# Performance work log

Hardware: AMD Instinct MI355X
Metric: run time of the kernel (lower is better)

The kernel has to match this reference:

```python
import jax, jax.numpy as jnp
import numpy as np

N = 4096   # query tokens
M = 4096   # key/value tokens
D = 512    # embedding_dim


def setup_inputs() -> dict:
    key = jax.random.key(0)
    kq, kk, kv = jax.random.split(key, 3)
    return {
        "query": jax.random.normal(kq, (N, D), dtype=jnp.float32),
        "key": jax.random.normal(kk, (M, D), dtype=jnp.float32),
        "value": jax.random.normal(kv, (M, D), dtype=jnp.float32),
    }


def reference(query, key, value):
    # scores = Q K^T  (no 1/sqrt(d) scaling in the original module)
    attention_scores = jnp.einsum("nd,md->nm", query, key)  # [N, M]
    attention_probs = jax.nn.softmax(attention_scores, axis=-1)  # [N, M]
    output = jnp.einsum("nm,md->nd", attention_probs, value)  # [N, D]
    return (output, attention_probs)
```

## Files before the change

kernel.cpp:

```cpp
#include <hip/hip_runtime.h>
#include <hip/hip_bf16.h>
#include <stdint.h>

#define N_Q 4096
#define N_K 4096
#define DIM 512

typedef float f32x4 __attribute__((ext_vector_type(4)));
typedef __bf16 bf16x8 __attribute__((ext_vector_type(8)));
typedef unsigned short u16x4 __attribute__((ext_vector_type(4)));
typedef int i32x4 __attribute__((ext_vector_type(4)));

__device__ __forceinline__ f32x4 mfma_bf16(bf16x8 a, bf16x8 b, f32x4 c) {
  return __builtin_amdgcn_mfma_f32_16x16x32_bf16(a, b, c, 0, 0, 0);
}

__device__ __forceinline__ i32x4 mfma_i8(i32x4 a, i32x4 b, i32x4 c) {
  return __builtin_amdgcn_mfma_i32_16x16x64_i8(a, b, c, 0, 0, 0);
}

__device__ __forceinline__ void gload16(const void* g, void* l) {
  __builtin_amdgcn_global_load_lds((const __attribute__((address_space(1))) void*)g,
                                   (__attribute__((address_space(3))) void*)l,
                                   16, 0, 0);
}

__device__ __forceinline__ void split4(const f32x4 v, u16x4& h, u16x4& l) {
#pragma unroll
  for (int i = 0; i < 4; ++i) {
    float f = v[i];
    uint32_t u = __builtin_bit_cast(uint32_t, f);
    uint32_t hb = (u + 0x8000u) & 0xffff0000u;
    float hf = __builtin_bit_cast(float, hb);
    float lf = f - hf;
    h[i] = (unsigned short)(hb >> 16);
    l[i] = (unsigned short)(__builtin_bit_cast(uint32_t, lf) >> 16);
  }
}

__device__ __forceinline__ unsigned short bf16r(float f) {
  uint32_t u = __builtin_bit_cast(uint32_t, f);
  return (unsigned short)((u + 0x8000u) >> 16);
}

__global__ __launch_bounds__(256) void prep_kernel(const float* __restrict__ Q,
                                                   const float* __restrict__ K,
                                                   const float* __restrict__ V,
                                                   signed char* __restrict__ Xq8,
                                                   signed char* __restrict__ Xk8,
                                                   float* __restrict__ sclA,
                                                   float* __restrict__ sclB,
                                                   unsigned short* __restrict__ Vt) {
  __shared__ unsigned short t[64][72];
  const int bid = blockIdx.x;
  const int tid = threadIdx.x;

  if (bid < 2048) {
    const bool isK = bid >= 1024;
    const float* X = isK ? K : Q;
    signed char* X8 = isK ? Xk8 : Xq8;
    float* scl = isK ? sclB : sclA;
    const int lane = tid & 63;
    const int row = (isK ? bid - 1024 : bid) * 4 + (tid >> 6);

    f32x4 v[2];
    v[0] = *(const f32x4*)(X + (size_t)row * DIM + lane * 8);
    v[1] = *(const f32x4*)(X + (size_t)row * DIM + lane * 8 + 4);

    float mx = 0.f;
#pragma unroll
    for (int u = 0; u < 2; ++u)
#pragma unroll
      for (int j = 0; j < 4; ++j) mx = fmaxf(mx, fabsf(v[u][j]));
#pragma unroll
    for (int o = 32; o > 0; o >>= 1) mx = fmaxf(mx, __shfl_xor(mx, o, 64));

    const float s = fmaxf(mx, 1e-20f) * (1.0f / 127.0f);
    const float rinv = 1.0f / s;
    const float linv = 128.0f * rinv;

    uint32_t hw[2], lw[2];
#pragma unroll
    for (int u = 0; u < 2; ++u) {
      uint32_t hword = 0, lword = 0;
#pragma unroll
      for (int j = 0; j < 4; ++j) {
        float x = v[u][j];
        int h = __float2int_rn(x * rinv);
        float r = x - s * (float)h;
        int l = __float2int_rn(r * linv);
        hword |= ((uint32_t)(h & 0xff)) << (8 * j);
        lword |= ((uint32_t)(l & 0xff)) << (8 * j);
      }
      hw[u] = hword; lw[u] = lword;
    }
    uint2 hv; hv.x = hw[0]; hv.y = hw[1];
    uint2 lv; lv.x = lw[0]; lv.y = lw[1];
    *(uint2*)(X8 + (size_t)row * 1024 + lane * 8) = hv;
    *(uint2*)(X8 + (size_t)row * 1024 + 512 + lane * 8) = lv;
    if (lane == 0) scl[row] = s;
  } else {
    const int b2 = bid - 2048;
    const int d0 = (b2 & 7) * 64;
    const int k0 = (b2 >> 3) * 64;
#pragma unroll
    for (int c = 0; c < 4; ++c) {
      int kr = (tid >> 4) + c * 16;
      f32x4 v = *(const f32x4*)(V + (size_t)(k0 + kr) * DIM + d0 + (tid & 15) * 4);
#pragma unroll
      for (int j = 0; j < 4; ++j) t[(tid & 15) * 4 + j][kr] = bf16r(v[j]);
    }
    __syncthreads();
#pragma unroll
    for (int c = 0; c < 2; ++c) {
      int d = (tid >> 3) + c * 32;
      int k = (tid & 7) * 8;
      *(uint4*)(Vt + (size_t)(d0 + d) * N_K + k0 + k) = *(const uint4*)&t[d][k];
    }
  }
}

__global__ __launch_bounds__(256, 2) void qk4_kernel(const signed char* __restrict__ Xq8,
                                                     const signed char* __restrict__ Xk8,
                                                     const float* __restrict__ sclA,
                                                     const float* __restrict__ sclB,
                                                     float* __restrict__ S) {
  __shared__ __align__(16) char smem[65536];

  const int tid = threadIdx.x;
  const int lane = tid & 63, wid = tid >> 6;
  const int wr = wid >> 1, wc = wid & 1;

  const int bid = blockIdx.x;
  const int b = (bid & 7) * 128 + (bid >> 3);
  const int rbase = (b >> 5) * 128;
  const int cbase = (b & 31) * 128;

  const int lrow = lane >> 3;
  const int lchk = lane & 7;

  const i32x4 izero = {0, 0, 0, 0};
  i32x4 acc_hh[4][4], acc_x[4][4];
#pragma unroll
  for (int m = 0; m < 4; ++m)
#pragma unroll
    for (int n = 0; n < 4; ++n) { acc_hh[m][n] = izero; acc_x[m][n] = izero; }

  auto stage = [&](int buf, int t) {
#pragma unroll
    for (int i = 0; i < 4; ++i) {
      const int r = (wid << 5) + (i << 3) + lrow;
      const int sc = lchk ^ (r & 7);
      const int colb = (sc < 4) ? (t * 64 + sc * 16) : (512 + t * 64 + (sc & 3) * 16);
      const signed char* g = Xq8 + (size_t)(rbase + r) * 1024 + colb;
      uint32_t off = (uint32_t)(buf * 32768 + (((wid << 5) + (i << 3)) << 7));
      off = (uint32_t)__builtin_amdgcn_readfirstlane((int)off);
      gload16(g, smem + off);
    }
#pragma unroll
    for (int i = 0; i < 4; ++i) {
      const int r = (wid << 5) + (i << 3) + lrow;
      const int sc = lchk ^ (r & 7);
      const int colb = (sc < 4) ? (t * 64 + sc * 16) : (512 + t * 64 + (sc & 3) * 16);
      const signed char* g = Xk8 + (size_t)(cbase + r) * 1024 + colb;
      uint32_t off = (uint32_t)(buf * 32768 + 16384 + (((wid << 5) + (i << 3)) << 7));
      off = (uint32_t)__builtin_amdgcn_readfirstlane((int)off);
      gload16(g, smem + off);
    }
  };

  auto compute = [&](int buf) {
    const char* bA = smem + buf * 32768;
    const char* bB = bA + 16384;
    const int kc = lane >> 4;
    i32x4 ah[4], al[4], bh[4], bl[4];
#pragma unroll
    for (int m = 0; m < 4; ++m) {
      int row = (wr << 6) + (m << 4) + (lane & 15);
      ah[m] = *(const i32x4*)(bA + row * 128 + ((kc ^ (row & 7)) << 4));
      al[m] = *(const i32x4*)(bA + row * 128 + (((4 + kc) ^ (row & 7)) << 4));
    }
#pragma unroll
    for (int n = 0; n < 4; ++n) {
      int row = (wc << 6) + (n << 4) + (lane & 15);
      bh[n] = *(const i32x4*)(bB + row * 128 + ((kc ^ (row & 7)) << 4));
      bl[n] = *(const i32x4*)(bB + row * 128 + (((4 + kc) ^ (row & 7)) << 4));
    }
    __builtin_amdgcn_s_setprio(1);
#pragma unroll
    for (int m = 0; m < 4; ++m)
#pragma unroll
      for (int n = 0; n < 4; ++n) {
        acc_hh[m][n] = mfma_i8(ah[m], bh[n], acc_hh[m][n]);
        acc_x[m][n]  = mfma_i8(ah[m], bl[n], acc_x[m][n]);
        acc_x[m][n]  = mfma_i8(al[m], bh[n], acc_x[m][n]);
      }
    __builtin_amdgcn_s_setprio(0);
  };

  stage(0, 0);
  stage(1, 1);
  for (int t = 0; t < 8; ++t) {
    if (t < 7) asm volatile("s_waitcnt vmcnt(8)" ::: "memory");
    else       asm volatile("s_waitcnt vmcnt(0)" ::: "memory");
    __builtin_amdgcn_s_barrier();
    compute(t & 1);
    asm volatile("s_waitcnt lgkmcnt(0)" ::: "memory");
    __builtin_amdgcn_sched_barrier(0);
    __builtin_amdgcn_s_barrier();
    if (t + 2 < 8) stage(t & 1, t + 2);
  }

#pragma unroll
  for (int m = 0; m < 4; ++m) {
    int row0 = rbase + wr * 64 + m * 16 + (lane >> 4) * 4;
    float sa[4];
#pragma unroll
    for (int j = 0; j < 4; ++j) sa[j] = sclA[row0 + j];
#pragma unroll
    for (int n = 0; n < 4; ++n) {
      int col = cbase + wc * 64 + n * 16 + (lane & 15);
      float sb = sclB[col];
#pragma unroll
      for (int j = 0; j < 4; ++j) {
        float f = (float)acc_hh[m][n][j] + (float)acc_x[m][n][j] * 0.0078125f;
        S[(size_t)(row0 + j) * N_K + col] = sa[j] * sb * f;
      }
    }
  }
}

__global__ __launch_bounds__(256, 2) void qk_kernel(const float* __restrict__ Q,
                                                    const float* __restrict__ K,
                                                    float* __restrict__ S) {
  __shared__ __align__(16) char sAh[16384];
  __shared__ __align__(16) char sAl[16384];
  __shared__ __align__(16) char sBh[16384];
  __shared__ __align__(16) char sBl[16384];

  const int tid = threadIdx.x;
  const int rbase = blockIdx.y * 128;
  const int cbase = blockIdx.x * 128;
  const int lane = tid & 63, wid = tid >> 6;
  const int wr = wid >> 1, wc = wid & 1;
  const int lr = lane & 15, lk = (lane >> 4) * 8;

  const int srow = tid >> 4;
  const int scol = (tid & 15) * 4;

  f32x4 qr[8], kr[8];
#pragma unroll
  for (int p = 0; p < 8; ++p) {
    int r = p * 16 + srow;
    qr[p] = *(const f32x4*)(Q + (size_t)(rbase + r) * DIM + scol);
    kr[p] = *(const f32x4*)(K + (size_t)(cbase + r) * DIM + scol);
  }

  const f32x4 fzero = {0.f, 0.f, 0.f, 0.f};
  f32x4 acc[4][4];
#pragma unroll
  for (int m = 0; m < 4; ++m)
#pragma unroll
    for (int n = 0; n < 4; ++n) acc[m][n] = fzero;

  for (int kk = 0; kk < DIM / 64; ++kk) {
    __syncthreads();
#pragma unroll
    for (int p = 0; p < 8; ++p) {
      int r = p * 16 + srow;
      uint32_t bo = (uint32_t)(r * 128) + (uint32_t)((scol * 2) ^ ((r & 7) << 4));
      u16x4 qh, ql, kh, kl;
      split4(qr[p], qh, ql);
      split4(kr[p], kh, kl);
      *(u16x4*)(sAh + bo) = qh;
      *(u16x4*)(sAl + bo) = ql;
      *(u16x4*)(sBh + bo) = kh;
      *(u16x4*)(sBl + bo) = kl;
    }
    __syncthreads();
    if (kk < DIM / 64 - 1) {
#pragma unroll
      for (int p = 0; p < 8; ++p) {
        int r = p * 16 + srow;
        qr[p] = *(const f32x4*)(Q + (size_t)(rbase + r) * DIM + (kk + 1) * 64 + scol);
        kr[p] = *(const f32x4*)(K + (size_t)(cbase + r) * DIM + (kk + 1) * 64 + scol);
      }
    }
#pragma unroll
    for (int kh = 0; kh < 2; ++kh) {
      bf16x8 a_h[4], a_l[4], b_h[4], b_l[4];
#pragma unroll
      for (int m = 0; m < 4; ++m) {
        int row = wr * 64 + m * 16 + lr;
        uint32_t co = (uint32_t)(((kh * 32 + lk) * 2) ^ ((row & 7) << 4));
        a_h[m] = *(const bf16x8*)(sAh + row * 128 + co);
        a_l[m] = *(const bf16x8*)(sAl + row * 128 + co);
      }
#pragma unroll
      for (int n = 0; n < 4; ++n) {
        int row = wc * 64 + n * 16 + lr;
        uint32_t co = (uint32_t)(((kh * 32 + lk) * 2) ^ ((row & 7) << 4));
        b_h[n] = *(const bf16x8*)(sBh + row * 128 + co);
        b_l[n] = *(const bf16x8*)(sBl + row * 128 + co);
      }
#pragma unroll
      for (int m = 0; m < 4; ++m)
#pragma unroll
        for (int n = 0; n < 4; ++n) {
          acc[m][n] = mfma_bf16(a_h[m], b_h[n], acc[m][n]);
          acc[m][n] = mfma_bf16(a_h[m], b_l[n], acc[m][n]);
          acc[m][n] = mfma_bf16(a_l[m], b_h[n], acc[m][n]);
        }
    }
  }

#pragma unroll
  for (int m = 0; m < 4; ++m) {
    int row = rbase + wr * 64 + m * 16 + (lane >> 4) * 4;
#pragma unroll
    for (int n = 0; n < 4; ++n) {
      int col = cbase + wc * 64 + n * 16 + lr;
#pragma unroll
      for (int j = 0; j < 4; ++j)
        S[(size_t)(row + j) * N_K + col] = acc[m][n][j];
    }
  }
}

__global__ __launch_bounds__(256) void softmax_kernel(float* __restrict__ P,
                                                      unsigned short* __restrict__ Pb) {
  const int tid = threadIdx.x;
  const int wid = tid >> 6, lane = tid & 63;
  float* p = P + (size_t)blockIdx.x * N_K;

  f32x4 v[4];
  float mx = -3.0e38f;
#pragma unroll
  for (int i = 0; i < 4; ++i) {
    v[i] = *(const f32x4*)(p + i * 1024 + tid * 4);
    mx = fmaxf(mx, fmaxf(fmaxf(v[i][0], v[i][1]), fmaxf(v[i][2], v[i][3])));
  }
#pragma unroll
  for (int o = 32; o > 0; o >>= 1) mx = fmaxf(mx, __shfl_xor(mx, o, 64));
  __shared__ float redM[4];
  __shared__ float redS[4];
  if (lane == 0) redM[wid] = mx;
  __syncthreads();
  mx = fmaxf(fmaxf(redM[0], redM[1]), fmaxf(redM[2], redM[3]));

  float s = 0.f;
#pragma unroll
  for (int i = 0; i < 4; ++i) {
#pragma unroll
    for (int j = 0; j < 4; ++j) {
      v[i][j] = __expf(v[i][j] - mx);
      s += v[i][j];
    }
  }
#pragma unroll
  for (int o = 32; o > 0; o >>= 1) s += __shfl_xor(s, o, 64);
  if (lane == 0) redS[wid] = s;
  __syncthreads();
  s = redS[0] + redS[1] + redS[2] + redS[3];
  const float inv = 1.0f / s;

  unsigned short* pb = Pb ? (Pb + (size_t)blockIdx.x * N_K) : nullptr;
#pragma unroll
  for (int i = 0; i < 4; ++i) {
    v[i] *= inv;
    *(f32x4*)(p + i * 1024 + tid * 4) = v[i];
    if (pb) {
      u16x4 h;
#pragma unroll
      for (int j = 0; j < 4; ++j) h[j] = bf16r(v[i][j]);
      *(u16x4*)(pb + i * 1024 + tid * 4) = h;
    }
  }
}

__global__ __launch_bounds__(256, 2) void pv5_kernel(const unsigned short* __restrict__ Pb,
                                                     const unsigned short* __restrict__ Vt,
                                                     float* __restrict__ Opart) {
  __shared__ __align__(16) char smem[65536];

  const int tid = threadIdx.x;
  const int lane = tid & 63, wid = tid >> 6;
  const int wr = wid >> 1, wc = wid & 1;
  const int rbase = blockIdx.y * 128;
  const int cbase = blockIdx.x * 128;
  const int k0 = blockIdx.z * 1024;
  float* Out = Opart + (size_t)blockIdx.z * ((size_t)N_Q * DIM);

  const int lrow = lane >> 3;
  const int lchk = lane & 7;

  const f32x4 fzero = {0.f, 0.f, 0.f, 0.f};
  f32x4 acc[4][4];
#pragma unroll
  for (int m = 0; m < 4; ++m)
#pragma unroll
    for (int n = 0; n < 4; ++n) acc[m][n] = fzero;

  auto stage = [&](int buf, int t) {
    const size_t kel = (size_t)k0 + ((size_t)t << 6);
#pragma unroll
    for (int i = 0; i < 4; ++i) {
      const int rr = (wid << 5) + (i << 3) + lrow;
      const int gc = lchk ^ (rr & 7);
      const void* gA = (const void*)(Pb + (size_t)(rbase + rr) * N_K + kel + (gc << 3));
      uint32_t off = (uint32_t)(buf * 32768 + (((wid << 5) + (i << 3)) << 7));
      off = (uint32_t)__builtin_amdgcn_readfirstlane((int)off);
      gload16(gA, smem + off);
    }
#pragma unroll
    for (int i = 0; i < 4; ++i) {
      const int rr = (wid << 5) + (i << 3) + lrow;
      const int gc = lchk ^ (rr & 7);
      const void* gB = (const void*)(Vt + (size_t)(cbase + rr) * N_K + kel + (gc << 3));
      uint32_t off = (uint32_t)(buf * 32768 + 16384 + (((wid << 5) + (i << 3)) << 7));
      off = (uint32_t)__builtin_amdgcn_readfirstlane((int)off);
      gload16(gB, smem + off);
    }
  };

  auto compute = [&](int buf) {
    const char* bA = smem + buf * 32768;
    const char* bB = bA + 16384;
#pragma unroll
    for (int kh = 0; kh < 2; ++kh) {
      bf16x8 a[4], bfr[4];
#pragma unroll
      for (int m = 0; m < 4; ++m) {
        int row = (wr << 6) + (m << 4) + (lane & 15);
        uint32_t co = (uint32_t)(((((kh << 2) + (lane >> 4)) << 4)) ^ ((row & 7) << 4));
        a[m] = *(const bf16x8*)(bA + row * 128 + co);
      }
#pragma unroll
      for (int n = 0; n < 4; ++n) {
        int row = (wc << 6) + (n << 4) + (lane & 15);
        uint32_t co = (uint32_t)(((((kh << 2) + (lane >> 4)) << 4)) ^ ((row & 7) << 4));
        bfr[n] = *(const bf16x8*)(bB + row * 128 + co);
      }
      __builtin_amdgcn_s_setprio(1);
#pragma unroll
      for (int m = 0; m < 4; ++m)
#pragma unroll
        for (int n = 0; n < 4; ++n)
          acc[m][n] = mfma_bf16(a[m], bfr[n], acc[m][n]);
      __builtin_amdgcn_s_setprio(0);
    }
  };

  stage(0, 0);
  stage(1, 1);
  for (int t = 0; t < 16; ++t) {
    if (t < 15) asm volatile("s_waitcnt vmcnt(8)" ::: "memory");
    else        asm volatile("s_waitcnt vmcnt(0)" ::: "memory");
    __builtin_amdgcn_s_barrier();
    compute(t & 1);
    asm volatile("s_waitcnt lgkmcnt(0)" ::: "memory");
    __builtin_amdgcn_sched_barrier(0);
    __builtin_amdgcn_s_barrier();
    if (t + 2 < 16) stage(t & 1, t + 2);
  }

#pragma unroll
  for (int m = 0; m < 4; ++m) {
    int row = rbase + wr * 64 + m * 16 + (lane >> 4) * 4;
#pragma unroll
    for (int n = 0; n < 4; ++n) {
      int col = cbase + wc * 64 + n * 16 + (lane & 15);
#pragma unroll
      for (int j = 0; j < 4; ++j)
        Out[(size_t)(row + j) * DIM + col] = acc[m][n][j];
    }
  }
}

__global__ __launch_bounds__(256) void reduce_kernel(float* __restrict__ O,
                                                     const float* __restrict__ Opart) {
  size_t i = ((size_t)blockIdx.x * 256 + threadIdx.x) * 4;
  f32x4 s = *(const f32x4*)(Opart + i);
#pragma unroll
  for (int z = 1; z < 4; ++z)
    s += *(const f32x4*)(Opart + (size_t)z * ((size_t)N_Q * DIM) + i);
  *(f32x4*)(O + i) = s;
}

__global__ __launch_bounds__(512, 2) void pv_kernel(const float* __restrict__ P,
                                                    const float* __restrict__ V,
                                                    float* __restrict__ O) {
  __shared__ __align__(16) char sA[16384];
  __shared__ __align__(16) char sB[16384];

  const int tid = threadIdx.x;
  const int rbase = blockIdx.y * 128;
  const int cbase = blockIdx.x * 128;
  const int lane = tid & 63, wid = tid >> 6;
  const int wr = wid >> 2, wc = wid & 3;
  const int lr = lane & 15, lk = (lane >> 4) * 8;

  const int a_row = tid >> 4;
  const int a_col = (tid & 15) * 4;
  const int b_c = tid & 127;
  const int b_oct = tid >> 7;

  f32x4 areg[4];
  float breg[4][4];
#pragma unroll
  for (int p = 0; p < 4; ++p) {
    int r = p * 32 + a_row;
    areg[p] = *(const f32x4*)(P + (size_t)(rbase + r) * N_K + a_col);
  }
#pragma unroll
  for (int g = 0; g < 4; ++g) {
    int kr0 = b_oct * 4 + g * 16;
#pragma unroll
    for (int i = 0; i < 4; ++i)
      breg[g][i] = V[(size_t)(kr0 + i) * DIM + cbase + b_c];
  }

  const f32x4 fzero = {0.f, 0.f, 0.f, 0.f};
  f32x4 acc[4][2];
#pragma unroll
  for (int m = 0; m < 4; ++m)
#pragma unroll
    for (int n = 0; n < 2; ++n) acc[m][n] = fzero;

  for (int kk = 0; kk < N_K / 64; ++kk) {
    __syncthreads();
#pragma unroll
    for (int p = 0; p < 4; ++p) {
      int r = p * 32 + a_row;
      uint32_t bo = (uint32_t)(r * 128) + (uint32_t)((a_col * 2) ^ ((r & 7) << 4));
      u16x4 hv;
#pragma unroll
      for (int i = 0; i < 4; ++i) hv[i] = bf16r(areg[p][i]);
      *(u16x4*)(sA + bo) = hv;
    }
#pragma unroll
    for (int g = 0; g < 4; ++g) {
      int kr0 = b_oct * 4 + g * 16;
      uint32_t bo = (uint32_t)(b_c * 128) + (uint32_t)((kr0 * 2) ^ ((b_c & 7) << 4));
      u16x4 hv;
#pragma unroll
      for (int i = 0; i < 4; ++i) hv[i] = bf16r(breg[g][i]);
      *(u16x4*)(sB + bo) = hv;
    }
    __syncthreads();
    if (kk < N_K / 64 - 1) {
#pragma unroll
      for (int p = 0; p < 4; ++p) {
        int r = p * 32 + a_row;
        areg[p] = *(const f32x4*)(P + (size_t)(rbase + r) * N_K + (kk + 1) * 64 + a_col);
      }
#pragma unroll
      for (int g = 0; g < 4; ++g) {
        int kr0 = b_oct * 4 + g * 16;
#pragma unroll
        for (int i = 0; i < 4; ++i)
          breg[g][i] = V[(size_t)((kk + 1) * 64 + kr0 + i) * DIM + cbase + b_c];
      }
    }
#pragma unroll
    for (int kh = 0; kh < 2; ++kh) {
      bf16x8 af[4], bf[2];
#pragma unroll
      for (int m = 0; m < 4; ++m) {
        int row = wr * 64 + m * 16 + lr;
        uint32_t co = (uint32_t)(((kh * 32 + lk) * 2) ^ ((row & 7) << 4));
        af[m] = *(const bf16x8*)(sA + row * 128 + co);
      }
#pragma unroll
      for (int n = 0; n < 2; ++n) {
        int row = wc * 32 + n * 16 + lr;
        uint32_t co = (uint32_t)(((kh * 32 + lk) * 2) ^ ((row & 7) << 4));
        bf[n] = *(const bf16x8*)(sB + row * 128 + co);
      }
#pragma unroll
      for (int m = 0; m < 4; ++m)
#pragma unroll
        for (int n = 0; n < 2; ++n)
          acc[m][n] = mfma_bf16(af[m], bf[n], acc[m][n]);
    }
  }

#pragma unroll
  for (int m = 0; m < 4; ++m) {
    int row = rbase + wr * 64 + m * 16 + (lane >> 4) * 4;
#pragma unroll
    for (int n = 0; n < 2; ++n) {
      int col = cbase + wc * 32 + n * 16 + lr;
#pragma unroll
      for (int j = 0; j < 4; ++j)
        O[(size_t)(row + j) * DIM + col] = acc[m][n][j];
    }
  }
}

extern "C" void kernel_launch(void* const* d_in, const int* in_sizes, int n_in,
                              void* d_out, int out_size, void* d_ws, size_t ws_size,
                              hipStream_t stream) {
  const float* Q = (const float*)d_in[0];
  const float* K = (const float*)d_in[1];
  const float* V = (const float*)d_in[2];
  float* O = (float*)d_out;
  float* P = O + (size_t)N_Q * DIM;

  const size_t PB_BYTES = (size_t)N_Q * N_K * 2;
  const size_t VT_BYTES = (size_t)DIM * N_K * 2;
  const size_t SCL_BYTES = 65536;
  const size_t OP_BYTES = (size_t)N_Q * DIM * 4;

  if (ws_size >= PB_BYTES + VT_BYTES + SCL_BYTES + 4 * OP_BYTES) {
    char* wsb = (char*)d_ws;
    signed char* Xq8 = (signed char*)wsb;
    signed char* Xk8 = Xq8 + (size_t)N_Q * 1024;
    unsigned short* Pb = (unsigned short*)wsb;
    unsigned short* Vt = (unsigned short*)(wsb + PB_BYTES);
    float* sclA = (float*)(wsb + PB_BYTES + VT_BYTES);
    float* sclB = sclA + N_Q;
    float* Opart = (float*)(wsb + PB_BYTES + VT_BYTES + SCL_BYTES);

    prep_kernel<<<2560, 256, 0, stream>>>(Q, K, V, Xq8, Xk8, sclA, sclB, Vt);
    qk4_kernel<<<1024, 256, 0, stream>>>(Xq8, Xk8, sclA, sclB, P);
    softmax_kernel<<<N_Q, 256, 0, stream>>>(P, Pb);
    pv5_kernel<<<dim3(DIM / 128, N_Q / 128, 4), 256, 0, stream>>>(Pb, Vt, Opart);
    reduce_kernel<<<(N_Q * DIM) / (256 * 4), 256, 0, stream>>>(O, Opart);
  } else {
    qk_kernel<<<dim3(N_K / 128, N_Q / 128), 256, 0, stream>>>(Q, K, P);
    softmax_kernel<<<N_Q, 256, 0, stream>>>(P, nullptr);
    pv_kernel<<<dim3(DIM / 128, N_Q / 128), 512, 0, stream>>>(P, V, O);
  }
}
```

Baseline: 114.4 us.

## Fuse softmax normalization into PV kernel using precomputed row statistics

Replaces the full softmax pass with a stats kernel that only computes per-row max and inverse sum. The PV kernel then reads raw fp32 scores, applies exp and normalization in registers, writes the fp32 probabilities from one column block, and stores bf16 tiles to LDS for the MFMA. This removes the separate write of normalized probabilities and the bf16 copy. In exchange the A operand now goes through registers rather than async LDS loads, fp32 reads are twice as wide, and exp is recomputed per column block.

New measurement: 142.9 us. 1.25x slower.

```diff
diff --git a/kernel.cpp b/kernel.cpp
--- a/kernel.cpp
+++ b/kernel.cpp
@@ -9,6 +9,7 @@
 typedef float f32x4 __attribute__((ext_vector_type(4)));
 typedef __bf16 bf16x8 __attribute__((ext_vector_type(8)));
 typedef unsigned short u16x4 __attribute__((ext_vector_type(4)));
+typedef unsigned short u16x8 __attribute__((ext_vector_type(8)));
 typedef int i32x4 __attribute__((ext_vector_type(4)));
 
 __device__ __forceinline__ f32x4 mfma_bf16(bf16x8 a, bf16x8 b, f32x4 c) {
@@ -230,6 +231,190 @@
   }
 }
 
+__global__ __launch_bounds__(256) void stats_kernel(const float* __restrict__ S,
+                                                    float* __restrict__ M,
+                                                    float* __restrict__ INV) {
+  const int tid = threadIdx.x;
+  const int wid = tid >> 6, lane = tid & 63;
+  const float* p = S + (size_t)blockIdx.x * N_K;
+
+  f32x4 v[4];
+  float mx = -3.0e38f;
+#pragma unroll
+  for (int i = 0; i < 4; ++i) {
+    v[i] = *(const f32x4*)(p + i * 1024 + tid * 4);
+    mx = fmaxf(mx, fmaxf(fmaxf(v[i][0], v[i][1]), fmaxf(v[i][2], v[i][3])));
+  }
+#pragma unroll
+  for (int o = 32; o > 0; o >>= 1) mx = fmaxf(mx, __shfl_xor(mx, o, 64));
+  __shared__ float redM[4];
+  __shared__ float redS[4];
+  if (lane == 0) redM[wid] = mx;
+  __syncthreads();
+  mx = fmaxf(fmaxf(redM[0], redM[1]), fmaxf(redM[2], redM[3]));
+
+  float s = 0.f;
+#pragma unroll
+  for (int i = 0; i < 4; ++i)
+#pragma unroll
+    for (int j = 0; j < 4; ++j) s += __expf(v[i][j] - mx);
+#pragma unroll
+  for (int o = 32; o > 0; o >>= 1) s += __shfl_xor(s, o, 64);
+  if (lane == 0) redS[wid] = s;
+  __syncthreads();
+  s = redS[0] + redS[1] + redS[2] + redS[3];
+
+  if (tid == 0) { M[blockIdx.x] = mx; INV[blockIdx.x] = 1.0f / s; }
+}
+
+__global__ __launch_bounds__(256, 2) void pvs_kernel(const float* __restrict__ S,
+                                                     const unsigned short* __restrict__ Vt,
+                                                     const float* __restrict__ M,
+                                                     const float* __restrict__ INV,
+                                                     float* __restrict__ P,
+                                                     float* __restrict__ Opart) {
+  __shared__ __align__(16) char smem[65536];
+
+  const int tid = threadIdx.x;
+  const int lane = tid & 63, wid = tid >> 6;
+  const int wr = wid >> 1, wc = wid & 1;
+  const int rbase = blockIdx.y * 128;
+  const int cbase = blockIdx.x * 128;
+  const int k0 = blockIdx.z * 1024;
+  const bool writeP = (blockIdx.x == 0);
+  float* Out = Opart + (size_t)blockIdx.z * ((size_t)N_Q * DIM);
+
+  const int gc = (lane & 7) ^ ((lane >> 3) & 7);
+  int rr_[4]; float m_[4], inv_[4];
+#pragma unroll
+  for (int i = 0; i < 4; ++i) {
+    rr_[i] = (wid << 5) + (i << 3) + (lane >> 3);
+    m_[i] = M[rbase + rr_[i]];
+    inv_[i] = INV[rbase + rr_[i]];
+  }
+
+  const f32x4 fzero = {0.f, 0.f, 0.f, 0.f};
+  f32x4 acc[4][4];
+#pragma unroll
+  for (int m = 0; m < 4; ++m)
+#pragma unroll
+    for (int n = 0; n < 4; ++n) acc[m][n] = fzero;
+
+  f32x4 rA[4][2];
+  auto loadA = [&](int t) {
+    const size_t kel = (size_t)k0 + ((size_t)t << 6) + (size_t)(gc << 3);
+#pragma unroll
+    for (int i = 0; i < 4; ++i) {
+      const float* g = S + (size_t)(rbase + rr_[i]) * N_K + kel;
+      rA[i][0] = *(const f32x4*)g;
+      rA[i][1] = *(const f32x4*)(g + 4);
+    }
+  };
+
+  auto stageB = [&](int buf, int t) {
+    const size_t kel = (size_t)k0 + ((size_t)t << 6);
+#pragma unroll
+    for (int i = 0; i < 4; ++i) {
+      const int rr = (wid << 5) + (i << 3) + (lane >> 3);
+      const int gcb = (lane & 7) ^ (rr & 7);
+      const void* g = (const void*)(Vt + (size_t)(cbase + rr) * N_K + kel + (gcb << 3));
+      uint32_t off = (uint32_t)(buf * 32768 + 16384 + (((wid << 5) + (i << 3)) << 7));
+      off = (uint32_t)__builtin_amdgcn_readfirstlane((int)off);
+      gload16(g, smem + off);
+    }
+  };
+
+  auto writeA = [&](int buf, int t) {
+    const size_t kel = (size_t)k0 + ((size_t)t << 6) + (size_t)(gc << 3);
+#pragma unroll
+    for (int i = 0; i < 4; ++i) {
+      f32x4 p0, p1;
+#pragma unroll
+      for (int j = 0; j < 4; ++j) {
+        p0[j] = __expf(rA[i][0][j] - m_[i]) * inv_[i];
+        p1[j] = __expf(rA[i][1][j] - m_[i]) * inv_[i];
+      }
+      if (writeP) {
+        float* gp = P + (size_t)(rbase + rr_[i]) * N_K + kel;
+        *(f32x4*)gp = p0;
+        *(f32x4*)(gp + 4) = p1;
+      }
+      u16x8 h;
+#pragma unroll
+      for (int j = 0; j < 4; ++j) { h[j] = bf16r(p0[j]); h[4 + j] = bf16r(p1[j]); }
+      *(u16x8*)(smem + buf * 32768 + (((wid << 5) + (i << 3)) << 7) + lane * 16) = h;
+    }
+  };
+
+  auto compute = [&](int buf) {
+    const char* bA = smem + buf * 32768;
+    const char* bB = bA + 16384;
+#pragma unroll
+    for (int kh = 0; kh < 2; ++kh) {
+      bf16x8 a[4], bfr[4];
+#pragma unroll
+      for (int m = 0; m < 4; ++m) {
+        int row = (wr << 6) + (m << 4) + (lane & 15);
+        uint32_t co = (uint32_t)(((((kh << 2) + (lane >> 4)) << 4)) ^ ((row & 7) << 4));
+        a[m] = *(const bf16x8*)(bA + row * 128 + co);
+      }
+#pragma unroll
+      for (int n = 0; n < 4; ++n) {
+        int row = (wc << 6) + (n << 4) + (lane & 15);
+        uint32_t co = (uint32_t)(((((kh << 2) + (lane >> 4)) << 4)) ^ ((row & 7) << 4));
+        bfr[n] = *(const bf16x8*)(bB + row * 128 + co);
+      }
+      __builtin_amdgcn_s_setprio(1);
+#pragma unroll
+      for (int m = 0; m < 4; ++m)
+#pragma unroll
+        for (int n = 0; n < 4; ++n)
+          acc[m][n] = mfma_bf16(a[m], bfr[n], acc[m][n]);
+      __builtin_amdgcn_s_setprio(0);
+    }
+  };
+
+  loadA(0);
+  stageB(0, 0);
+  asm volatile("s_waitcnt vmcnt(0)" ::: "memory");
+  writeA(0, 0);
+  __syncthreads();
+
+  int cur = 0;
+  for (int t = 0; t < 16; ++t) {
+    if (t + 1 < 16) { loadA(t + 1); stageB(cur ^ 1, t + 1); }
+    compute(cur);
+    if (t + 1 < 16) {
+      asm volatile("s_waitcnt vmcnt(4)" ::: "memory");
+      writeA(cur ^ 1, t + 1);
+    }
+    __syncthreads();
+    cur ^= 1;
+  }
+
+#pragma unroll
+  for (int m = 0; m < 4; ++m) {
+    int row = rbase + wr * 64 + m * 16 + (lane >> 4) * 4;
+#pragma unroll
+    for (int n = 0; n < 4; ++n) {
+      int col = cbase + wc * 64 + n * 16 + (lane & 15);
+#pragma unroll
+      for (int j = 0; j < 4; ++j)
+        Out[(size_t)(row + j) * DIM + col] = acc[m][n][j];
+    }
+  }
+}
+
+__global__ __launch_bounds__(256) void reduce_kernel(float* __restrict__ O,
+                                                     const float* __restrict__ Opart) {
+  size_t i = ((size_t)blockIdx.x * 256 + threadIdx.x) * 4;
+  f32x4 s = *(const f32x4*)(Opart + i);
+#pragma unroll
+  for (int z = 1; z < 4; ++z)
+    s += *(const f32x4*)(Opart + (size_t)z * ((size_t)N_Q * DIM) + i);
+  *(f32x4*)(O + i) = s;
+}
+
 __global__ __launch_bounds__(256, 2) void qk_kernel(const float* __restrict__ Q,
                                                     const float* __restrict__ K,
                                                     float* __restrict__ S) {
@@ -327,8 +512,7 @@
   }
 }
 
-__global__ __launch_bounds__(256) void softmax_kernel(float* __restrict__ P,
-                                                      unsigned short* __restrict__ Pb) {
+__global__ __launch_bounds__(256) void softmax_kernel(float* __restrict__ P) {
   const int tid = threadIdx.x;
   const int wid = tid >> 6, lane = tid & 63;
   float* p = P + (size_t)blockIdx.x * N_K;
@@ -350,141 +534,23 @@
 
   float s = 0.f;
 #pragma unroll
-  for (int i = 0; i < 4; ++i) {
+  for (int i = 0; i < 4; ++i)
 #pragma unroll
     for (int j = 0; j < 4; ++j) {
       v[i][j] = __expf(v[i][j] - mx);
       s += v[i][j];
     }
-  }
 #pragma unroll
   for (int o = 32; o > 0; o >>= 1) s += __shfl_xor(s, o, 64);
   if (lane == 0) redS[wid] = s;
   __syncthreads();
   s = redS[0] + redS[1] + redS[2] + redS[3];
   const float inv = 1.0f / s;
-
-  unsigned short* pb = Pb ? (Pb + (size_t)blockIdx.x * N_K) : nullptr;
 #pragma unroll
   for (int i = 0; i < 4; ++i) {
     v[i] *= inv;
     *(f32x4*)(p + i * 1024 + tid * 4) = v[i];
-    if (pb) {
-      u16x4 h;
-#pragma unroll
-      for (int j = 0; j < 4; ++j) h[j] = bf16r(v[i][j]);
-      *(u16x4*)(pb + i * 1024 + tid * 4) = h;
-    }
-  }
-}
-
-__global__ __launch_bounds__(256, 2) void pv5_kernel(const unsigned short* __restrict__ Pb,
-                                                     const unsigned short* __restrict__ Vt,
-                                                     float* __restrict__ Opart) {
-  __shared__ __align__(16) char smem[65536];
-
-  const int tid = threadIdx.x;
-  const int lane = tid & 63, wid = tid >> 6;
-  const int wr = wid >> 1, wc = wid & 1;
-  const int rbase = blockIdx.y * 128;
-  const int cbase = blockIdx.x * 128;
-  const int k0 = blockIdx.z * 1024;
-  float* Out = Opart + (size_t)blockIdx.z * ((size_t)N_Q * DIM);
-
-  const int lrow = lane >> 3;
-  const int lchk = lane & 7;
-
-  const f32x4 fzero = {0.f, 0.f, 0.f, 0.f};
-  f32x4 acc[4][4];
-#pragma unroll
-  for (int m = 0; m < 4; ++m)
-#pragma unroll
-    for (int n = 0; n < 4; ++n) acc[m][n] = fzero;
-
-  auto stage = [&](int buf, int t) {
-    const size_t kel = (size_t)k0 + ((size_t)t << 6);
-#pragma unroll
-    for (int i = 0; i < 4; ++i) {
-      const int rr = (wid << 5) + (i << 3) + lrow;
-      const int gc = lchk ^ (rr & 7);
-      const void* gA = (const void*)(Pb + (size_t)(rbase + rr) * N_K + kel + (gc << 3));
-      uint32_t off = (uint32_t)(buf * 32768 + (((wid << 5) + (i << 3)) << 7));
-      off = (uint32_t)__builtin_amdgcn_readfirstlane((int)off);
-      gload16(gA, smem + off);
-    }
-#pragma unroll
-    for (int i = 0; i < 4; ++i) {
-      const int rr = (wid << 5) + (i << 3) + lrow;
-      const int gc = lchk ^ (rr & 7);
-      const void* gB = (const void*)(Vt + (size_t)(cbase + rr) * N_K + kel + (gc << 3));
-      uint32_t off = (uint32_t)(buf * 32768 + 16384 + (((wid << 5) + (i << 3)) << 7));
-      off = (uint32_t)__builtin_amdgcn_readfirstlane((int)off);
-      gload16(gB, smem + off);
-    }
-  };
-
-  auto compute = [&](int buf) {
-    const char* bA = smem + buf * 32768;
-    const char* bB = bA + 16384;
-#pragma unroll
-    for (int kh = 0; kh < 2; ++kh) {
-      bf16x8 a[4], bfr[4];
-#pragma unroll
-      for (int m = 0; m < 4; ++m) {
-        int row = (wr << 6) + (m << 4) + (lane & 15);
-        uint32_t co = (uint32_t)(((((kh << 2) + (lane >> 4)) << 4)) ^ ((row & 7) << 4));
-        a[m] = *(const bf16x8*)(bA + row * 128 + co);
-      }
-#pragma unroll
-      for (int n = 0; n < 4; ++n) {
-        int row = (wc << 6) + (n << 4) + (lane & 15);
-        uint32_t co = (uint32_t)(((((kh << 2) + (lane >> 4)) << 4)) ^ ((row & 7) << 4));
-        bfr[n] = *(const bf16x8*)(bB + row * 128 + co);
-      }
-      __builtin_amdgcn_s_setprio(1);
-#pragma unroll
-      for (int m = 0; m < 4; ++m)
-#pragma unroll
-        for (int n = 0; n < 4; ++n)
-          acc[m][n] = mfma_bf16(a[m], bfr[n], acc[m][n]);
-      __builtin_amdgcn_s_setprio(0);
-    }
-  };
-
-  stage(0, 0);
-  stage(1, 1);
-  for (int t = 0; t < 16; ++t) {
-    if (t < 15) asm volatile("s_waitcnt vmcnt(8)" ::: "memory");
-    else        asm volatile("s_waitcnt vmcnt(0)" ::: "memory");
-    __builtin_amdgcn_s_barrier();
-    compute(t & 1);
-    asm volatile("s_waitcnt lgkmcnt(0)" ::: "memory");
-    __builtin_amdgcn_sched_barrier(0);
-    __builtin_amdgcn_s_barrier();
-    if (t + 2 < 16) stage(t & 1, t + 2);
-  }
-
-#pragma unroll
-  for (int m = 0; m < 4; ++m) {
-    int row = rbase + wr * 64 + m * 16 + (lane >> 4) * 4;
-#pragma unroll
-    for (int n = 0; n < 4; ++n) {
-      int col = cbase + wc * 64 + n * 16 + (lane & 15);
-#pragma unroll
-      for (int j = 0; j < 4; ++j)
-        Out[(size_t)(row + j) * DIM + col] = acc[m][n][j];
-    }
-  }
-}
-
-__global__ __launch_bounds__(256) void reduce_kernel(float* __restrict__ O,
-                                                     const float* __restrict__ Opart) {
-  size_t i = ((size_t)blockIdx.x * 256 + threadIdx.x) * 4;
-  f32x4 s = *(const f32x4*)(Opart + i);
-#pragma unroll
-  for (int z = 1; z < 4; ++z)
-    s += *(const f32x4*)(Opart + (size_t)z * ((size_t)N_Q * DIM) + i);
-  *(f32x4*)(O + i) = s;
+  }
 }
 
 __global__ __launch_bounds__(512, 2) void pv_kernel(const float* __restrict__ P,
@@ -607,29 +673,32 @@
   float* O = (float*)d_out;
   float* P = O + (size_t)N_Q * DIM;
 
-  const size_t PB_BYTES = (size_t)N_Q * N_K * 2;
+  const size_t S_BYTES = (size_t)N_Q * N_K * 4;
   const size_t VT_BYTES = (size_t)DIM * N_K * 2;
   const size_t SCL_BYTES = 65536;
   const size_t OP_BYTES = (size_t)N_Q * DIM * 4;
-
-  if (ws_size >= PB_BYTES + VT_BYTES + SCL_BYTES + 4 * OP_BYTES) {
+  const size_t X8_BYTES = (size_t)N_Q * 1024;
+
+  if (ws_size >= S_BYTES + VT_BYTES + SCL_BYTES + 4 * OP_BYTES + 2 * X8_BYTES) {
     char* wsb = (char*)d_ws;
-    signed char* Xq8 = (signed char*)wsb;
-    signed char* Xk8 = Xq8 + (size_t)N_Q * 1024;
-    unsigned short* Pb = (unsigned short*)wsb;
-    unsigned short* Vt = (unsigned short*)(wsb + PB_BYTES);
-    float* sclA = (float*)(wsb + PB_BYTES + VT_BYTES);
+    float* Sws = (float*)wsb;
+    unsigned short* Vt = (unsigned short*)(wsb + S_BYTES);
+    float* sclA = (float*)(wsb + S_BYTES + VT_BYTES);
     float* sclB = sclA + N_Q;
-    float* Opart = (float*)(wsb + PB_BYTES + VT_BYTES + SCL_BYTES);
+    float* Mrow = sclB + N_Q;
+    float* INVrow = Mrow + N_Q;
+    float* Opart = (float*)(wsb + S_BYTES + VT_BYTES + SCL_BYTES);
+    signed char* Xq8 = (signed char*)(wsb + S_BYTES + VT_BYTES + SCL_BYTES + 4 * OP_BYTES);
+    signed char* Xk8 = Xq8 + X8_BYTES;
 
     prep_kernel<<<2560, 256, 0, stream>>>(Q, K, V, Xq8, Xk8, sclA, sclB, Vt);
-    qk4_kernel<<<1024, 256, 0, stream>>>(Xq8, Xk8, sclA, sclB, P);
-    softmax_kernel<<<N_Q, 256, 0, stream>>>(P, Pb);
-    pv5_kernel<<<dim3(DIM / 128, N_Q / 128, 4), 256, 0, stream>>>(Pb, Vt, Opart);
+    qk4_kernel<<<1024, 256, 0, stream>>>(Xq8, Xk8, sclA, sclB, Sws);
+    stats_kernel<<<N_Q, 256, 0, stream>>>(Sws, Mrow, INVrow);
+    pvs_kernel<<<dim3(DIM / 128, N_Q / 128, 4), 256, 0, stream>>>(Sws, Vt, Mrow, INVrow, P, Opart);
     reduce_kernel<<<(N_Q * DIM) / (256 * 4), 256, 0, stream>>>(O, Opart);
   } else {
     qk_kernel<<<dim3(N_K / 128, N_Q / 128), 256, 0, stream>>>(Q, K, P);
-    softmax_kernel<<<N_Q, 256, 0, stream>>>(P, nullptr);
+    softmax_kernel<<<N_Q, 256, 0, stream>>>(P);
     pv_kernel<<<dim3(DIM / 128, N_Q / 128), 512, 0, stream>>>(P, V, O);
   }
 }
```

## Enlarge QK int8 tile to 256x128 with 8 waves sharing K tile

Applied to the files above, without the earlier changes.

The QK score kernel now runs 512-thread blocks over 256x128 output tiles, so each staged K tile is reused by twice as many query rows. Shared memory grows to 96KB, the staging indexing is rewritten and the wait count is adjusted. The softmax kernel drops its null check on the bf16 output, and a separate fallback softmax is added for the small-workspace path. This adds register and LDS pressure that may limit occupancy to one block per CU.

Measured after the change: 114.2 us. Within noise of the previous version (-0.2%).

```diff
diff --git a/kernel.cpp b/kernel.cpp
--- a/kernel.cpp
+++ b/kernel.cpp
@@ -120,24 +120,21 @@
   }
 }
 
-__global__ __launch_bounds__(256, 2) void qk4_kernel(const signed char* __restrict__ Xq8,
+__global__ __launch_bounds__(512, 2) void qk5_kernel(const signed char* __restrict__ Xq8,
                                                      const signed char* __restrict__ Xk8,
                                                      const float* __restrict__ sclA,
                                                      const float* __restrict__ sclB,
                                                      float* __restrict__ S) {
-  __shared__ __align__(16) char smem[65536];
+  __shared__ __align__(16) char smem[98304];
 
   const int tid = threadIdx.x;
   const int lane = tid & 63, wid = tid >> 6;
   const int wr = wid >> 1, wc = wid & 1;
 
   const int bid = blockIdx.x;
-  const int b = (bid & 7) * 128 + (bid >> 3);
-  const int rbase = (b >> 5) * 128;
+  const int b = (bid & 7) * 64 + (bid >> 3);
+  const int rbase = (b >> 5) * 256;
   const int cbase = (b & 31) * 128;
-
-  const int lrow = lane >> 3;
-  const int lchk = lane & 7;
 
   const i32x4 izero = {0, 0, 0, 0};
   i32x4 acc_hh[4][4], acc_x[4][4];
@@ -147,31 +144,30 @@
     for (int n = 0; n < 4; ++n) { acc_hh[m][n] = izero; acc_x[m][n] = izero; }
 
   auto stage = [&](int buf, int t) {
+    const int rsub = tid >> 3;
+    const int sc = (lane & 7) ^ ((lane >> 3) & 7);
+    const int colb = (sc < 4) ? (t * 64 + sc * 16) : (512 + t * 64 + (sc & 3) * 16);
 #pragma unroll
     for (int i = 0; i < 4; ++i) {
-      const int r = (wid << 5) + (i << 3) + lrow;
-      const int sc = lchk ^ (r & 7);
-      const int colb = (sc < 4) ? (t * 64 + sc * 16) : (512 + t * 64 + (sc & 3) * 16);
+      const int r = i * 64 + rsub;
       const signed char* g = Xq8 + (size_t)(rbase + r) * 1024 + colb;
-      uint32_t off = (uint32_t)(buf * 32768 + (((wid << 5) + (i << 3)) << 7));
+      uint32_t off = (uint32_t)(buf * 49152 + ((i * 64 + wid * 8) << 7));
       off = (uint32_t)__builtin_amdgcn_readfirstlane((int)off);
       gload16(g, smem + off);
     }
 #pragma unroll
-    for (int i = 0; i < 4; ++i) {
-      const int r = (wid << 5) + (i << 3) + lrow;
-      const int sc = lchk ^ (r & 7);
-      const int colb = (sc < 4) ? (t * 64 + sc * 16) : (512 + t * 64 + (sc & 3) * 16);
+    for (int i = 0; i < 2; ++i) {
+      const int r = i * 64 + rsub;
       const signed char* g = Xk8 + (size_t)(cbase + r) * 1024 + colb;
-      uint32_t off = (uint32_t)(buf * 32768 + 16384 + (((wid << 5) + (i << 3)) << 7));
+      uint32_t off = (uint32_t)(buf * 49152 + 32768 + ((i * 64 + wid * 8) << 7));
       off = (uint32_t)__builtin_amdgcn_readfirstlane((int)off);
       gload16(g, smem + off);
     }
   };
 
   auto compute = [&](int buf) {
-    const char* bA = smem + buf * 32768;
-    const char* bB = bA + 16384;
+    const char* bA = smem + buf * 49152;
+    const char* bB = bA + 32768;
     const int kc = lane >> 4;
     i32x4 ah[4], al[4], bh[4], bl[4];
 #pragma unroll
@@ -201,7 +197,7 @@
   stage(0, 0);
   stage(1, 1);
   for (int t = 0; t < 8; ++t) {
-    if (t < 7) asm volatile("s_waitcnt vmcnt(8)" ::: "memory");
+    if (t < 7) asm volatile("s_waitcnt vmcnt(6)" ::: "memory");
     else       asm volatile("s_waitcnt vmcnt(0)" ::: "memory");
     __builtin_amdgcn_s_barrier();
     compute(t & 1);
@@ -364,17 +360,15 @@
   s = redS[0] + redS[1] + redS[2] + redS[3];
   const float inv = 1.0f / s;
 
-  unsigned short* pb = Pb ? (Pb + (size_t)blockIdx.x * N_K) : nullptr;
+  unsigned short* pb = Pb + (size_t)blockIdx.x * N_K;
 #pragma unroll
   for (int i = 0; i < 4; ++i) {
     v[i] *= inv;
     *(f32x4*)(p + i * 1024 + tid * 4) = v[i];
-    if (pb) {
-      u16x4 h;
-#pragma unroll
-      for (int j = 0; j < 4; ++j) h[j] = bf16r(v[i][j]);
-      *(u16x4*)(pb + i * 1024 + tid * 4) = h;
-    }
+    u16x4 h;
+#pragma unroll
+    for (int j = 0; j < 4; ++j) h[j] = bf16r(v[i][j]);
+    *(u16x4*)(pb + i * 1024 + tid * 4) = h;
   }
 }
 
@@ -487,6 +481,47 @@
   *(f32x4*)(O + i) = s;
 }
 
+__global__ __launch_bounds__(256) void softmax_fb_kernel(float* __restrict__ P) {
+  const int tid = threadIdx.x;
+  const int wid = tid >> 6, lane = tid & 63;
+  float* p = P + (size_t)blockIdx.x * N_K;
+
+  f32x4 v[4];
+  float mx = -3.0e38f;
+#pragma unroll
+  for (int i = 0; i < 4; ++i) {
+    v[i] = *(const f32x4*)(p + i * 1024 + tid * 4);
+    mx = fmaxf(mx, fmaxf(fmaxf(v[i][0], v[i][1]), fmaxf(v[i][2], v[i][3])));
+  }
+#pragma unroll
+  for (int o = 32; o > 0; o >>= 1) mx = fmaxf(mx, __shfl_xor(mx, o, 64));
+  __shared__ float redM[4];
+  __shared__ float redS[4];
+  if (lane == 0) redM[wid] = mx;
+  __syncthreads();
+  mx = fmaxf(fmaxf(redM[0], redM[1]), fmaxf(redM[2], redM[3]));
+
+  float s = 0.f;
+#pragma unroll
+  for (int i = 0; i < 4; ++i)
+#pragma unroll
+    for (int j = 0; j < 4; ++j) {
+      v[i][j] = __expf(v[i][j] - mx);
+      s += v[i][j];
+    }
+#pragma unroll
+  for (int o = 32; o > 0; o >>= 1) s += __shfl_xor(s, o, 64);
+  if (lane == 0) redS[wid] = s;
+  __syncthreads();
+  s = redS[0] + redS[1] + redS[2] + redS[3];
+  const float inv = 1.0f / s;
+#pragma unroll
+  for (int i = 0; i < 4; ++i) {
+    v[i] *= inv;
+    *(f32x4*)(p + i * 1024 + tid * 4) = v[i];
+  }
+}
+
 __global__ __launch_bounds__(512, 2) void pv_kernel(const float* __restrict__ P,
                                                     const float* __restrict__ V,
                                                     float* __restrict__ O) {
@@ -623,13 +658,13 @@
     float* Opart = (float*)(wsb + PB_BYTES + VT_BYTES + SCL_BYTES);
 
     prep_kernel<<<2560, 256, 0, stream>>>(Q, K, V, Xq8, Xk8, sclA, sclB, Vt);
-    qk4_kernel<<<1024, 256, 0, stream>>>(Xq8, Xk8, sclA, sclB, P);
+    qk5_kernel<<<512, 512, 0, stream>>>(Xq8, Xk8, sclA, sclB, P);
     softmax_kernel<<<N_Q, 256, 0, stream>>>(P, Pb);
     pv5_kernel<<<dim3(DIM / 128, N_Q / 128, 4), 256, 0, stream>>>(Pb, Vt, Opart);
     reduce_kernel<<<(N_Q * DIM) / (256 * 4), 256, 0, stream>>>(O, Opart);
   } else {
     qk_kernel<<<dim3(N_K / 128, N_Q / 128), 256, 0, stream>>>(Q, K, P);
-    softmax_kernel<<<N_Q, 256, 0, stream>>>(P, nullptr);
+    softmax_fb_kernel<<<N_Q, 256, 0, stream>>>(P);
     pv_kernel<<<dim3(DIM / 128, N_Q / 128), 512, 0, stream>>>(P, V, O);
   }
 }
```
